# Kernel tuning notes

Measured on AMD Instinct MI355X. Metric: run time of the kernel, lower is better.

The kernel has to match this reference:

```python
import jax, jax.numpy as jnp
import numpy as np
from jax import lax

NUM_ITER = 10      # max_num_iter
DAMP = 1.0         # bp_dumping_rate


def setup_inputs() -> dict:
    key = jax.random.key(0)
    k1, k2 = jax.random.split(key)
    N = 50000
    E = 800000   # undirected edges; 2E directed messages
    Q = 8
    edge_index = jax.random.randint(k1, (2, E), 0, N, dtype=jnp.int32)
    psi0 = jax.random.uniform(k2, (2 * E, Q), dtype=jnp.float32)
    beta = jnp.ones((1,), dtype=jnp.float32)
    return {"edge_index": edge_index, "psi0": psi0, "beta": beta, "num_nodes": N}


def _bp(edge_index, psi0, beta, num_nodes):
    Q = psi0.shape[1]
    E = edge_index.shape[1]
    src_u = edge_index[0]
    dst_u = edge_index[1]
    # directed edge list: e in [0,E) is u->v, e+E is v->u; rev maps each edge to its reverse
    src = jnp.concatenate([src_u, dst_u])            # [2E]
    dst = jnp.concatenate([dst_u, src_u])            # [2E]
    rev = jnp.concatenate([jnp.arange(E, 2 * E), jnp.arange(0, E)])
    b = beta[0]
    w = jnp.exp(b) - 1.0                              # e^beta - 1
    psi = jax.nn.softmax(psi0, axis=-1)               # init_bp: normalized random messages

    def node_field(psi):
        log_term = jnp.log1p(w * psi)                 # [2E, Q]
        node_sum = jax.ops.segment_sum(log_term, dst, num_segments=num_nodes)  # [N, Q]
        return log_term, node_sum

    def step(psi, _):
        log_term, node_sum = node_field(psi)
        marginal = jax.nn.softmax(node_sum, axis=-1)  # [N, Q]
        h = (b / num_nodes) * marginal.sum(axis=0)    # external mean field [Q]
        # message i->j: cavity = full incoming field at i minus contribution of j->i
        logits = node_sum[src] - log_term[rev] - h    # [2E, Q]
        new_psi = jax.nn.softmax(logits, axis=-1)
        max_diff = jnp.max(jnp.abs(new_psi - psi))
        psi = DAMP * new_psi + (1.0 - DAMP) * psi
        return psi, max_diff

    psi, diffs = lax.scan(step, psi, None, length=NUM_ITER)
    _, node_sum = node_field(psi)
    marginal = jax.nn.softmax(node_sum, axis=-1)
    return psi, marginal


def reference(edge_index, psi0, beta, num_nodes):
    message_map, marginal_psi = _bp(edge_index, psi0, beta, num_nodes)
    return message_map, marginal_psi
```

## Files before the change

### kernel.cpp

```cpp
#include <hip/hip_runtime.h>

#define QD 8
#define BLK 256
#define NBIN 1024

typedef unsigned short u16;
typedef unsigned int   u32;

__device__ __forceinline__ float bf2f(u16 u) {
    return __uint_as_float(((u32)u) << 16);
}
__device__ __forceinline__ u16 f2bf(float f) {
    u32 x = __float_as_uint(f);
    return (u16)((x + 0x7FFFu + ((x >> 16) & 1u)) >> 16);
}

__device__ __forceinline__ void load8(const float* __restrict__ p, float v[QD]) {
    const float4* p4 = reinterpret_cast<const float4*>(p);
    float4 a = p4[0], b = p4[1];
    v[0]=a.x; v[1]=a.y; v[2]=a.z; v[3]=a.w;
    v[4]=b.x; v[5]=b.y; v[6]=b.z; v[7]=b.w;
}
__device__ __forceinline__ void store8(float* __restrict__ p, const float v[QD]) {
    float4* p4 = reinterpret_cast<float4*>(p);
    float4 a = {v[0],v[1],v[2],v[3]};
    float4 b = {v[4],v[5],v[6],v[7]};
    p4[0]=a; p4[1]=b;
}
__device__ __forceinline__ void loadbf8(const u16* __restrict__ p, float v[QD]) {
    uint4 u = *reinterpret_cast<const uint4*>(p);
    v[0]=bf2f(u.x & 0xffff); v[1]=bf2f(u.x >> 16);
    v[2]=bf2f(u.y & 0xffff); v[3]=bf2f(u.y >> 16);
    v[4]=bf2f(u.z & 0xffff); v[5]=bf2f(u.z >> 16);
    v[6]=bf2f(u.w & 0xffff); v[7]=bf2f(u.w >> 16);
}
__device__ __forceinline__ void storebf8(u16* __restrict__ p, const float v[QD]) {
    uint4 u;
    u.x = (u32)f2bf(v[0]) | ((u32)f2bf(v[1]) << 16);
    u.y = (u32)f2bf(v[2]) | ((u32)f2bf(v[3]) << 16);
    u.z = (u32)f2bf(v[4]) | ((u32)f2bf(v[5]) << 16);
    u.w = (u32)f2bf(v[6]) | ((u32)f2bf(v[7]) << 16);
    *reinterpret_cast<uint4*>(p) = u;
}

__device__ __forceinline__ void softmax8(const float v[QD], float o[QD]) {
    float m = v[0];
    #pragma unroll
    for (int i=1;i<QD;i++) m = fmaxf(m, v[i]);
    float s = 0.f;
    #pragma unroll
    for (int i=0;i<QD;i++){ o[i] = __expf(v[i]-m); s += o[i]; }
    float inv = 1.0f/s;
    #pragma unroll
    for (int i=0;i<QD;i++) o[i] *= inv;
}

__global__ void count_kernel(const int* __restrict__ ei, int* __restrict__ deg, int twoE) {
    int x = blockIdx.x*BLK + threadIdx.x;
    if (x >= twoE) return;
    atomicAdd(&deg[ei[x]], 1);
}

__global__ void scan_kernel(const int* __restrict__ deg, int* __restrict__ rowstart,
                            int* __restrict__ cursor, int N, int twoE) {
    __shared__ int part[1024];
    int tid = threadIdx.x;
    int chunk = (N + 1023) / 1024;
    int lo = tid * chunk;
    int hi = lo + chunk; if (hi > N) hi = N; if (lo > N) lo = N;
    int s = 0;
    for (int i = lo; i < hi; ++i) s += deg[i];
    part[tid] = s;
    __syncthreads();
    for (int off = 1; off < 1024; off <<= 1) {
        int v = (tid >= off) ? part[tid - off] : 0;
        __syncthreads();
        part[tid] += v;
        __syncthreads();
    }
    int run = (tid == 0) ? 0 : part[tid - 1];
    for (int i = lo; i < hi; ++i) {
        rowstart[i] = run; cursor[i] = run; run += deg[i];
    }
    if (tid == 1023) rowstart[N] = twoE;
}

__global__ void histo_kernel(const int* __restrict__ deg, int* __restrict__ histo, int N) {
    int n = blockIdx.x*BLK + threadIdx.x;
    if (n >= N) return;
    int b = deg[n]; if (b > NBIN-1) b = NBIN-1;
    atomicAdd(&histo[b], 1);
}

__global__ void hscan_kernel(const int* __restrict__ histo, int* __restrict__ hcur) {
    __shared__ int part[NBIN];
    int tid = threadIdx.x;
    part[tid] = histo[tid];
    __syncthreads();
    for (int off = 1; off < NBIN; off <<= 1) {
        int v = (tid >= off) ? part[tid - off] : 0;
        __syncthreads();
        part[tid] += v;
        __syncthreads();
    }
    hcur[tid] = (tid == 0) ? 0 : part[tid - 1];
}

__global__ void order_kernel(const int* __restrict__ deg, int* __restrict__ hcur,
                             int* __restrict__ order, int N) {
    int n = blockIdx.x*BLK + threadIdx.x;
    if (n >= N) return;
    int b = deg[n]; if (b > NBIN-1) b = NBIN-1;
    int pos = atomicAdd(&hcur[b], 1);
    order[pos] = n;
}

__global__ void fill_kernel(const int* __restrict__ ei, const float* __restrict__ psi0,
                            int* __restrict__ cursor, int* __restrict__ adj,
                            u16* __restrict__ psi, int E, int twoE) {
    int e = blockIdx.x*BLK + threadIdx.x;
    if (e >= twoE) return;
    int r = (e < E) ? (e + E) : (e - E);
    int d = ei[r];
    int slot = atomicAdd(&cursor[d], 1);
    adj[slot] = e;
    float v[QD], o[QD];
    load8(psi0 + (size_t)e*QD, v);
    softmax8(v, o);
    storebf8(psi + (size_t)e*QD, o);
}

template<bool FINAL>
__global__ void nodesumA(const u16* __restrict__ psi, const int* __restrict__ adj,
                         const int* __restrict__ rowstart, const int* __restrict__ order,
                         float* __restrict__ ns, float* __restrict__ hslot,
                         float* __restrict__ marg,
                         const float* __restrict__ beta, int N) {
    int gid = blockIdx.x*BLK + threadIdx.x;
    int g = gid >> 3;
    int q = gid & 7;
    float w = __expf(beta[0]) - 1.0f;
    float hc = 0.0f;
    if (g < N) {
        int node = order[g];
        int s = rowstart[node], t = rowstart[node + 1];
        float acc = 0.0f;
        int i = s;
        for (; i + 16 <= t; i += 16) {
            int e[16];
            #pragma unroll
            for (int k = 0; k < 16; ++k) e[k] = adj[i + k];
            u16 a[16];
            #pragma unroll
            for (int k = 0; k < 16; ++k) a[k] = psi[(size_t)e[k]*QD + q];
            #pragma unroll
            for (int k = 0; k < 16; ++k) acc += __logf(fmaf(w, bf2f(a[k]), 1.0f));
        }
        for (; i + 4 <= t; i += 4) {
            int e[4];
            #pragma unroll
            for (int k = 0; k < 4; ++k) e[k] = adj[i + k];
            u16 a[4];
            #pragma unroll
            for (int k = 0; k < 4; ++k) a[k] = psi[(size_t)e[k]*QD + q];
            #pragma unroll
            for (int k = 0; k < 4; ++k) acc += __logf(fmaf(w, bf2f(a[k]), 1.0f));
        }
        for (; i < t; ++i)
            acc += __logf(fmaf(w, bf2f(psi[(size_t)adj[i]*QD + q]), 1.0f));

        float m = acc;
        #pragma unroll
        for (int d = 1; d < 8; d <<= 1) m = fmaxf(m, __shfl_xor(m, d, 8));
        float ex = __expf(acc - m);
        float ss = ex;
        #pragma unroll
        for (int d = 1; d < 8; d <<= 1) ss += __shfl_xor(ss, d, 8);
        if (FINAL) {
            marg[(size_t)node*QD + q] = ex / ss;
        } else {
            ns[(size_t)node*QD + q] = acc;
            hc = ex / ss;
        }
    }
    if (!FINAL) {
        hc += __shfl_xor(hc, 8);
        hc += __shfl_xor(hc, 16);
        hc += __shfl_xor(hc, 32);
        if ((threadIdx.x & 63) < 8) unsafeAtomicAdd(&hslot[threadIdx.x & 7], hc);
    }
}

template<bool LAST>
__global__ void pair_update(u16* __restrict__ psi, const int* __restrict__ ei,
                            const float* __restrict__ ns, const float* __restrict__ hslot,
                            float* __restrict__ out, const float* __restrict__ beta,
                            int E, float invN) {
    int t = blockIdx.x*BLK + threadIdx.x;
    if (t >= E) return;
    float b = beta[0];
    float w = __expf(b) - 1.0f;
    float hb = b * invN;
    int u = ei[t];
    int v = ei[t + E];
    float pf[QD], pr[QD], nsu[QD], nsv[QD], lg[QD], of_[QD], or_[QD], h8[QD];
    loadbf8(psi + (size_t)t*QD, pf);
    loadbf8(psi + ((size_t)t + E)*QD, pr);
    load8(ns + (size_t)u*QD, nsu);
    load8(ns + (size_t)v*QD, nsv);
    #pragma unroll
    for (int q = 0; q < QD; q++) h8[q] = hb * hslot[q];
    #pragma unroll
    for (int q = 0; q < QD; q++) lg[q] = nsu[q] - __logf(fmaf(w, pr[q], 1.0f)) - h8[q];
    softmax8(lg, of_);
    #pragma unroll
    for (int q = 0; q < QD; q++) lg[q] = nsv[q] - __logf(fmaf(w, pf[q], 1.0f)) - h8[q];
    softmax8(lg, or_);
    storebf8(psi + (size_t)t*QD, of_);
    storebf8(psi + ((size_t)t + E)*QD, or_);
    if (LAST) {
        store8(out + (size_t)t*QD, of_);
        store8(out + ((size_t)t + E)*QD, or_);
    }
}

extern "C" void kernel_launch(void* const* d_in, const int* in_sizes, int n_in,
                              void* d_out, int out_size, void* d_ws, size_t ws_size,
                              hipStream_t stream) {
    const int*   ei   = (const int*)d_in[0];
    const float* psi0 = (const float*)d_in[1];
    const float* beta = (const float*)d_in[2];

    int twoE = in_sizes[0];
    int E    = twoE / 2;
    int N    = (out_size - in_sizes[1]) / QD;

    char* w = (char*)d_ws;
    size_t o = 0;
    auto al = [](size_t x){ return (x + 255) & ~(size_t)255; };
    u16*  psi    = (u16*)(w + o);   o = al(o + (size_t)twoE*QD*2);
    int*  adj    = (int*)(w + o);   o = al(o + (size_t)twoE*4);
    float* ns    = (float*)(w + o); o = al(o + (size_t)N*QD*4);
    int*  deg    = (int*)(w + o);   o = al(o + (size_t)N*4);
    int*  rowstart=(int*)(w + o);   o = al(o + ((size_t)N+1)*4);
    int*  cursor = (int*)(w + o);   o = al(o + (size_t)N*4);
    int*  order  = (int*)(w + o);   o = al(o + (size_t)N*4);
    int*  histo  = (int*)(w + o);   o = al(o + (size_t)NBIN*4);
    int*  hcur   = (int*)(w + o);   o = al(o + (size_t)NBIN*4);
    float* hsl   = (float*)(w + o);

    int eg2 = (twoE + BLK - 1) / BLK;
    int eg1 = (E    + BLK - 1) / BLK;
    int ng8 = (N*QD + BLK - 1) / BLK;
    int ng  = (N    + BLK - 1) / BLK;
    float invN = 1.0f / (float)N;
    float* out = (float*)d_out;

    hipMemsetAsync(deg,   0, (size_t)N * sizeof(int), stream);
    hipMemsetAsync(histo, 0, (size_t)NBIN * sizeof(int), stream);
    hipMemsetAsync(hsl,   0, (size_t)11 * QD * sizeof(float), stream);

    count_kernel<<<eg2, BLK, 0, stream>>>(ei, deg, twoE);
    scan_kernel<<<1, 1024, 0, stream>>>(deg, rowstart, cursor, N, twoE);
    histo_kernel<<<ng, BLK, 0, stream>>>(deg, histo, N);
    hscan_kernel<<<1, NBIN, 0, stream>>>(histo, hcur);
    order_kernel<<<ng, BLK, 0, stream>>>(deg, hcur, order, N);
    fill_kernel<<<eg2, BLK, 0, stream>>>(ei, psi0, cursor, adj, psi, E, twoE);

    for (int k = 0; k < 10; ++k) {
        nodesumA<false><<<ng8, BLK, 0, stream>>>(psi, adj, rowstart, order, ns,
                                                 hsl + k*QD, nullptr, beta, N);
        if (k < 9)
            pair_update<false><<<eg1, BLK, 0, stream>>>(psi, ei, ns, hsl + k*QD,
                                                        out, beta, E, invN);
        else
            pair_update<true><<<eg1, BLK, 0, stream>>>(psi, ei, ns, hsl + k*QD,
                                                       out, beta, E, invN);
    }
    nodesumA<true><<<ng8, BLK, 0, stream>>>(psi, adj, rowstart, order, ns,
                                            hsl + 10*QD, out + (size_t)twoE*QD, beta, N);
}
```

Before: 1.698 ms.

## Parallelize CSR row-offset scan across blocks and shrink degree histogram

Replaces the single-block serial-chunk prefix scan over node degrees with a three-kernel multi-block scan (per-block scan, scan of block sums, add-back). Each thread of the old kernel walked about 49 degrees sequentially, twice. The degree histogram bin count is cut from 1024 to 256, and the psi gather index is computed in 32-bit before widening. The change adds two extra kernel launches, and degrees of 255 or more now fall into one ordering bin.

```diff
diff --git a/kernel.cpp b/kernel.cpp
--- a/kernel.cpp
+++ b/kernel.cpp
@@ -2,7 +2,7 @@
 
 #define QD 8
 #define BLK 256
-#define NBIN 1024
+#define NBIN 256
 
 typedef unsigned short u16;
 typedef unsigned int   u32;
@@ -61,28 +61,48 @@
     atomicAdd(&deg[ei[x]], 1);
 }
 
-__global__ void scan_kernel(const int* __restrict__ deg, int* __restrict__ rowstart,
-                            int* __restrict__ cursor, int N, int twoE) {
-    __shared__ int part[1024];
-    int tid = threadIdx.x;
-    int chunk = (N + 1023) / 1024;
-    int lo = tid * chunk;
-    int hi = lo + chunk; if (hi > N) hi = N; if (lo > N) lo = N;
-    int s = 0;
-    for (int i = lo; i < hi; ++i) s += deg[i];
-    part[tid] = s;
+__global__ void scan1_kernel(const int* __restrict__ deg, int* __restrict__ local,
+                             int* __restrict__ bsum, int N) {
+    __shared__ int sh[BLK];
+    int n = blockIdx.x*BLK + threadIdx.x;
+    int v = (n < N) ? deg[n] : 0;
+    sh[threadIdx.x] = v;
+    __syncthreads();
+    #pragma unroll
+    for (int off = 1; off < BLK; off <<= 1) {
+        int t = (threadIdx.x >= off) ? sh[threadIdx.x - off] : 0;
+        __syncthreads();
+        sh[threadIdx.x] += t;
+        __syncthreads();
+    }
+    if (n < N) local[n] = sh[threadIdx.x] - v;
+    if (threadIdx.x == BLK-1) bsum[blockIdx.x] = sh[BLK-1];
+}
+
+__global__ void scan2_kernel(int* __restrict__ bsum, int nb) {
+    __shared__ int sh[1024];
+    int t = threadIdx.x;
+    int v = (t < nb) ? bsum[t] : 0;
+    sh[t] = v;
     __syncthreads();
     for (int off = 1; off < 1024; off <<= 1) {
-        int v = (tid >= off) ? part[tid - off] : 0;
-        __syncthreads();
-        part[tid] += v;
-        __syncthreads();
-    }
-    int run = (tid == 0) ? 0 : part[tid - 1];
-    for (int i = lo; i < hi; ++i) {
-        rowstart[i] = run; cursor[i] = run; run += deg[i];
-    }
-    if (tid == 1023) rowstart[N] = twoE;
+        int x = (t >= off) ? sh[t - off] : 0;
+        __syncthreads();
+        sh[t] += x;
+        __syncthreads();
+    }
+    if (t < nb) bsum[t] = sh[t] - v;
+}
+
+__global__ void scan3_kernel(const int* __restrict__ bsum, int* __restrict__ local_cursor,
+                             int* __restrict__ rowstart, int N, int twoE) {
+    int n = blockIdx.x*BLK + threadIdx.x;
+    if (n < N) {
+        int r = local_cursor[n] + bsum[blockIdx.x];
+        rowstart[n] = r;
+        local_cursor[n] = r;
+    }
+    if (n == 0) rowstart[N] = twoE;
 }
 
 __global__ void histo_kernel(const int* __restrict__ deg, int* __restrict__ histo, int N) {
@@ -152,7 +172,7 @@
             for (int k = 0; k < 16; ++k) e[k] = adj[i + k];
             u16 a[16];
             #pragma unroll
-            for (int k = 0; k < 16; ++k) a[k] = psi[(size_t)e[k]*QD + q];
+            for (int k = 0; k < 16; ++k) a[k] = psi[(size_t)((u32)e[k]*QD + q)];
             #pragma unroll
             for (int k = 0; k < 16; ++k) acc += __logf(fmaf(w, bf2f(a[k]), 1.0f));
         }
@@ -162,12 +182,12 @@
             for (int k = 0; k < 4; ++k) e[k] = adj[i + k];
             u16 a[4];
             #pragma unroll
-            for (int k = 0; k < 4; ++k) a[k] = psi[(size_t)e[k]*QD + q];
+            for (int k = 0; k < 4; ++k) a[k] = psi[(size_t)((u32)e[k]*QD + q)];
             #pragma unroll
             for (int k = 0; k < 4; ++k) acc += __logf(fmaf(w, bf2f(a[k]), 1.0f));
         }
         for (; i < t; ++i)
-            acc += __logf(fmaf(w, bf2f(psi[(size_t)adj[i]*QD + q]), 1.0f));
+            acc += __logf(fmaf(w, bf2f(psi[(size_t)((u32)adj[i]*QD + q)]), 1.0f));
 
         float m = acc;
         #pragma unroll
@@ -247,6 +267,7 @@
     int*  order  = (int*)(w + o);   o = al(o + (size_t)N*4);
     int*  histo  = (int*)(w + o);   o = al(o + (size_t)NBIN*4);
     int*  hcur   = (int*)(w + o);   o = al(o + (size_t)NBIN*4);
+    int*  bsum   = (int*)(w + o);   o = al(o + (size_t)1024*4);
     float* hsl   = (float*)(w + o);
 
     int eg2 = (twoE + BLK - 1) / BLK;
@@ -261,7 +282,9 @@
     hipMemsetAsync(hsl,   0, (size_t)11 * QD * sizeof(float), stream);
 
     count_kernel<<<eg2, BLK, 0, stream>>>(ei, deg, twoE);
-    scan_kernel<<<1, 1024, 0, stream>>>(deg, rowstart, cursor, N, twoE);
+    scan1_kernel<<<ng, BLK, 0, stream>>>(deg, cursor, bsum, N);
+    scan2_kernel<<<1, 1024, 0, stream>>>(bsum, ng);
+    scan3_kernel<<<ng, BLK, 0, stream>>>(bsum, cursor, rowstart, N, twoE);
     histo_kernel<<<ng, BLK, 0, stream>>>(deg, histo, N);
     hscan_kernel<<<1, NBIN, 0, stream>>>(histo, hcur);
     order_kernel<<<ng, BLK, 0, stream>>>(deg, hcur, order, N);
```

Result: faster. 1.613 ms (-5.0%).
